# Performance work log

Measured on AMD Instinct MI355X. Metric: run time of the kernel, lower is better.

## Reference

```python
import jax, jax.numpy as jnp
import numpy as np

EMBED_DIM = 768
ATTN_DIM = 64


def setup_inputs() -> dict:
    key = jax.random.key(0)
    k1, k2, k3, k4 = jax.random.split(key, 4)
    embedded = jax.random.normal(k1, (4, 4096, EMBED_DIM), dtype=jnp.float32)
    scale = 1.0 / np.sqrt(EMBED_DIM)
    Wq = jax.random.normal(k2, (EMBED_DIM, ATTN_DIM), dtype=jnp.float32) * scale
    Wk = jax.random.normal(k3, (EMBED_DIM, ATTN_DIM), dtype=jnp.float32) * scale
    Wv = jax.random.normal(k4, (EMBED_DIM, ATTN_DIM), dtype=jnp.float32) * scale
    return {"embedded": embedded, "Wq": Wq, "Wk": Wk, "Wv": Wv}


def reference(embedded, Wq, Wk, Wv):
    # Linear projections (bias=False): [B, S, A]
    q = jnp.einsum("bse,ea->bsa", embedded, Wq)
    k = jnp.einsum("bse,ea->bsa", embedded, Wk)
    v = jnp.einsum("bse,ea->bsa", embedded, Wv)
    # Full [B, S, S] score matrix, as in the original naive implementation
    scores = jnp.einsum("bqa,bka->bqk", q, k) / jnp.sqrt(jnp.float32(ATTN_DIM))
    seq_len = embedded.shape[-2]
    causal = jnp.tril(jnp.ones((seq_len, seq_len), dtype=bool))
    scores = jnp.where(causal, scores, -jnp.inf)
    weights = jax.nn.softmax(scores, axis=-1)
    output = jnp.einsum("bqk,bka->bqa", weights, v)
    # torch.round(output, decimals=4)
    return jnp.round(output * 1e4) / 1e4
```

## Files before the change

### kernel.cpp

```cpp
#include <hip/hip_runtime.h>

#define NB 4
#define SEQ 4096
#define EMB 768
#define AD 64
#define BS (NB*SEQ)
#define CHK 16

typedef short short8 __attribute__((ext_vector_type(8)));
typedef float f32x4 __attribute__((ext_vector_type(4)));
typedef int   i32x2 __attribute__((ext_vector_type(2)));
typedef unsigned short u16;

__device__ __forceinline__ u16 f2bf(float f) {
  union { float f; unsigned u; } v; v.f = f;
  unsigned u = v.u;
  unsigned r = (u + 0x7FFFu + ((u >> 16) & 1u)) >> 16;
  return (u16)r;
}

__device__ __forceinline__ float bf2f(u16 b) {
  union { unsigned u; float f; } v; v.u = ((unsigned)b) << 16;
  return v.f;
}

__device__ __forceinline__ unsigned cvt_pk_bf16(float lo, float hi) {
  unsigned r;
  asm("v_cvt_pk_bf16_f32 %0, %1, %2" : "=v"(r) : "v"(lo), "v"(hi));
  return r;
}

__device__ __forceinline__ f32x4 mfma16(short8 a, short8 b, f32x4 c) {
  return __builtin_amdgcn_mfma_f32_16x16x32_bf16(a, b, c, 0, 0, 0);
}

__device__ __forceinline__ void gload16(const u16* g, u16* l) {
  __builtin_amdgcn_global_load_lds(
      (const __attribute__((address_space(1))) unsigned*)g,
      (__attribute__((address_space(3))) unsigned*)l, 16, 0, 0);
}

__device__ __forceinline__ float xor16_max(float x) {
#if __has_builtin(__builtin_amdgcn_permlane16_swap)
  i32x2 r = __builtin_amdgcn_permlane16_swap(__float_as_int(x), __float_as_int(x), false, false);
  return fmaxf(__int_as_float(r[0]), __int_as_float(r[1]));
#else
  return fmaxf(x, __shfl_xor(x, 16));
#endif
}
__device__ __forceinline__ float xor16_sum(float x) {
#if __has_builtin(__builtin_amdgcn_permlane16_swap)
  i32x2 r = __builtin_amdgcn_permlane16_swap(__float_as_int(x), __float_as_int(x), false, false);
  return __int_as_float(r[0]) + __int_as_float(r[1]);
#else
  return x + __shfl_xor(x, 16);
#endif
}
__device__ __forceinline__ float xor32_max(float x) {
#if __has_builtin(__builtin_amdgcn_permlane32_swap)
  i32x2 r = __builtin_amdgcn_permlane32_swap(__float_as_int(x), __float_as_int(x), false, false);
  return fmaxf(__int_as_float(r[0]), __int_as_float(r[1]));
#else
  return fmaxf(x, __shfl_xor(x, 32));
#endif
}
__device__ __forceinline__ float xor32_sum(float x) {
#if __has_builtin(__builtin_amdgcn_permlane32_swap)
  i32x2 r = __builtin_amdgcn_permlane32_swap(__float_as_int(x), __float_as_int(x), false, false);
  return __int_as_float(r[0]) + __int_as_float(r[1]);
#else
  return x + __shfl_xor(x, 32);
#endif
}

__global__ void wt_kernel(const float* __restrict__ Wq, const float* __restrict__ Wk,
                          const float* __restrict__ Wv, u16* __restrict__ Wt) {
  int idx = blockIdx.x * 256 + threadIdx.x;
  if (idx >= 3 * AD * EMB) return;
  int m   = idx / (AD * EMB);
  int rem = idx - m * (AD * EMB);
  int col = rem / EMB;
  int e   = rem - col * EMB;
  const float* W = (m == 0) ? Wq : (m == 1) ? Wk : Wv;
  Wt[idx] = f2bf(W[e * AD + col]);
}

__global__ __launch_bounds__(512) void proj_kernel(const float* __restrict__ emb,
                                                   const u16* __restrict__ Wt,
                                                   u16* __restrict__ Q, u16* __restrict__ K,
                                                   u16* __restrict__ Vt) {
  const int w = threadIdx.x >> 6;
  const int lane = threadIdx.x & 63;
  const int g = lane >> 4, c = lane & 15;
  const int wr = w & 1;
  const int cq = w >> 1;
  const int rbase = blockIdx.x * 32;

  __shared__ __align__(16) char ebuf[2][2][4096];
  __shared__ __align__(16) char wbuf[2][2][12288];
  __shared__ u16 t[32][65];

  const int r8 = lane >> 3, j8 = lane & 7;
  const int c4 = lane >> 2, j4 = lane & 3;

  f32x4 acc[3];
#pragma unroll
  for (int fi = 0; fi < 3; ++fi)
#pragma unroll
    for (int r = 0; r < 4; ++r) acc[fi][r] = 0.f;

#define PSTAGE(bufi, kk, kt) do {                                              \
    { const int col = w * 16 + c4;                                             \
      const int kc = (col & 3) ^ ((col >> 2) & 3);                             \
      gload16(Wt + (size_t)col * EMB + (kt) * 32 + ((j4 ^ kc) << 3),           \
              (u16*)(wbuf[bufi][kk] + w * 1024)); }                            \
    if (w < 4) {                                                               \
      gload16((const u16*)(emb + (size_t)(rbase + w * 8 + r8) * EMB            \
                           + (kt) * 32 + ((j8 ^ r8) << 2)),                    \
              (u16*)(ebuf[bufi][kk] + w * 1024));                              \
    } else {                                                                   \
      const int col = (4 + w) * 16 + c4;                                       \
      const int kc = (col & 3) ^ ((col >> 2) & 3);                             \
      gload16(Wt + (size_t)col * EMB + (kt) * 32 + ((j4 ^ kc) << 3),           \
              (u16*)(wbuf[bufi][kk] + (4 + w) * 1024));                        \
    }                                                                          \
  } while (0)

  PSTAGE(0, 0, 0);
  PSTAGE(0, 1, 1);
  __syncthreads();

  int cur = 0;
  for (int it = 0; it < 12; ++it) {
    if (it + 1 < 12) {
      PSTAGE(cur ^ 1, 0, 2 * it + 2);
      PSTAGE(cur ^ 1, 1, 2 * it + 3);
    }

#pragma unroll
    for (int kk = 0; kk < 2; ++kk) {
      const char* eb = ebuf[cur][kk];
      const int arow = (wr * 16 + c) * 128;
      const int sw = (c & 7) << 4;
      float4 fa0 = *(const float4*)(eb + arow + ((g * 32) ^ sw));
      float4 fa1 = *(const float4*)(eb + arow + ((g * 32 + 16) ^ sw));
      union { unsigned u[4]; short8 v; } uu;
      uu.u[0] = cvt_pk_bf16(fa0.x, fa0.y);
      uu.u[1] = cvt_pk_bf16(fa0.z, fa0.w);
      uu.u[2] = cvt_pk_bf16(fa1.x, fa1.y);
      uu.u[3] = cvt_pk_bf16(fa1.z, fa1.w);
      const short8 af = uu.v;

      const char* wb = wbuf[cur][kk];
#pragma unroll
      for (int fi = 0; fi < 3; ++fi) {
        const int fg = cq * 3 + fi;
        const int col = (fg >> 2) * 64 + (fg & 3) * 16 + c;
        const int kc = (col & 3) ^ ((col >> 2) & 3);
        short8 bf = *(const short8*)(wb + col * 64 + ((g ^ kc) << 4));
        acc[fi] = mfma16(af, bf, acc[fi]);
      }
    }

    __syncthreads();
    cur ^= 1;
  }

#pragma unroll
  for (int fi = 0; fi < 3; ++fi) {
    const int fg = cq * 3 + fi;
    const int m = fg >> 2, cf = fg & 3;
    const int col = cf * 16 + c;
#pragma unroll
    for (int r = 0; r < 4; ++r) {
      const int rloc = wr * 16 + g * 4 + r;
      const size_t grow = (size_t)(rbase + rloc);
      const float v = acc[fi][r];
      if (m == 0)      Q[grow * AD + col] = f2bf(v * 0.125f);
      else if (m == 1) K[grow * AD + col] = f2bf(v);
      else             t[rloc][col] = f2bf(v);
    }
  }
  __syncthreads();
  const int bb = blockIdx.x >> 7;
  const int sb = (blockIdx.x & 127) * 32;
  const int s = threadIdx.x & 31;
  const int d0 = threadIdx.x >> 5;
#pragma unroll
  for (int it = 0; it < 4; ++it) {
    const int d = it * 16 + d0;
    Vt[(size_t)(bb * AD + d) * SEQ + sb + s] = t[s][d];
  }
#undef PSTAGE
}

__global__ __launch_bounds__(256, 3) void flash_part(const u16* __restrict__ Q,
                                                     const u16* __restrict__ K,
                                                     const u16* __restrict__ Vt,
                                                     u16* __restrict__ opart,
                                                     float* __restrict__ ml) {
  const int bx = blockIdx.x;
  const int b = bx & 3;
  const int u = bx >> 2;
  int bq, c;
  if (u < 16)       { bq = 16 + u;        c = 0; }
  else if (u < 32)  { bq = 32 + (u - 16); c = 0; }
  else if (u < 48)  { bq = 32 + (u - 32); c = 1; }
  else if (u < 64)  { bq = 48 + (u - 48); c = 0; }
  else if (u < 80)  { bq = 48 + (u - 64); c = 1; }
  else if (u < 96)  { bq = 48 + (u - 80); c = 2; }
  else { int d = u - 96; bq = (d >> 4) * 16 + 15 - (d & 15); c = d >> 4; }
  const int t0 = c * CHK;
  const int tend = (c == (bq >> 4)) ? (bq + 1) : (t0 + CHK);

  const int w = threadIdx.x >> 6;
  const int lane = threadIdx.x & 63;
  const int g = lane >> 4, cl = lane & 15;
  const int r8 = lane >> 3, c16 = lane & 7;
  const int q0 = bq * 64 + w * 16;

  const u16* Qb = Q + (size_t)b * SEQ * AD;
  const u16* Kb = K + (size_t)b * SEQ * AD;
  const u16* Vb = Vt + (size_t)b * AD * SEQ;

  __shared__ __align__(16) u16 kbuf[2][64 * 64];
  __shared__ __align__(16) u16 vbuf[2][64 * 64];
  __shared__ __align__(16) u16 plds_all[4][16 * 64];
  char* plds = (char*)plds_all[w];
  const int swz = (cl & 7) << 4;
  const int prow = cl * 128;
  const int fsw = (cl & 7);

  const short8 qf0 = *(const short8*)(Qb + (size_t)(q0 + cl) * AD + g * 8);
  const short8 qf1 = *(const short8*)(Qb + (size_t)(q0 + cl) * AD + 32 + g * 8);

  float mrow = -INFINITY, lrow = 0.f;
  f32x4 o[4];
#pragma unroll
  for (int cf = 0; cf < 4; cf++)
#pragma unroll
    for (int r = 0; r < 4; r++) o[cf][r] = 0.f;

#define STAGE(bufi, tt) do {                                                   \
    const int kvb = (tt) * 64;                                                 \
    const int row0 = w * 16 + r8, row1 = w * 16 + 8 + r8;                      \
    gload16(Kb + (size_t)(kvb + row0) * AD + ((c16 ^ r8) << 3),                \
            &kbuf[bufi][(w * 16) * 64]);                                       \
    gload16(Kb + (size_t)(kvb + row1) * AD + ((c16 ^ r8) << 3),                \
            &kbuf[bufi][(w * 16 + 8) * 64]);                                   \
    gload16(Vb + (size_t)row0 * SEQ + kvb + ((c16 ^ r8) << 3),                 \
            &vbuf[bufi][(w * 16) * 64]);                                       \
    gload16(Vb + (size_t)row1 * SEQ + kvb + ((c16 ^ r8) << 3),                 \
            &vbuf[bufi][(w * 16 + 8) * 64]);                                   \
  } while (0)

  STAGE(0, t0);
  __syncthreads();

  int cur = 0;
  for (int t = t0; t < tend; ++t) {
    const int kv0 = t * 64;
    if (t + 1 < tend) STAGE(cur ^ 1, t + 1);

    const char* kb = (const char*)kbuf[cur];
    const char* vb = (const char*)vbuf[cur];

    short8 kf0[4], kf1[4];
#pragma unroll
    for (int cf = 0; cf < 4; cf++) {
      const int kr = (cf * 16 + cl) * 128;
      kf0[cf] = *(const short8*)(kb + kr + ((g ^ fsw) << 4));
      kf1[cf] = *(const short8*)(kb + kr + (((4 + g) ^ fsw) << 4));
    }

    f32x4 s4[4];
#pragma unroll
    for (int cf = 0; cf < 4; cf++) {
      f32x4 z; z[0] = z[1] = z[2] = z[3] = 0.f;
      z = mfma16(kf0[cf], qf0, z);
      s4[cf] = mfma16(kf1[cf], qf1, z);
    }

    if (t == bq) {
#pragma unroll
      for (int cf = 0; cf < 4; cf++) {
        const int kvb2 = kv0 + cf * 16 + g * 4;
#pragma unroll
        for (int r = 0; r < 4; r++)
          s4[cf][r] = (kvb2 + r <= q0 + cl) ? s4[cf][r] : -INFINITY;
      }
    }

    float tm[4];
#pragma unroll
    for (int cf = 0; cf < 4; cf++)
      tm[cf] = fmaxf(fmaxf(s4[cf][0], s4[cf][1]), fmaxf(s4[cf][2], s4[cf][3]));
    float mt = fmaxf(fmaxf(tm[0], tm[1]), fmaxf(tm[2], tm[3]));
    mt = xor16_max(mt);
    mt = xor32_max(mt);

    if (!__all(mt <= mrow + 8.0f)) {
      const float mn = fmaxf(mrow, mt);
      const float corr = __expf(mrow - mn);
      mrow = mn;
      lrow *= corr;
      float cb[4];
#pragma unroll
      for (int r = 0; r < 4; r++) cb[r] = __shfl(corr, g * 20 + r);
#pragma unroll
      for (int cf = 0; cf < 4; cf++) {
        o[cf][0] *= cb[0]; o[cf][1] *= cb[1];
        o[cf][2] *= cb[2]; o[cf][3] *= cb[3];
      }
    }

    float rs = 0.f;
#pragma unroll
    for (int cf = 0; cf < 4; cf++) {
      const float p0 = __expf(s4[cf][0] - mrow);
      const float p1 = __expf(s4[cf][1] - mrow);
      const float p2 = __expf(s4[cf][2] - mrow);
      const float p3 = __expf(s4[cf][3] - mrow);
      rs += (p0 + p1) + (p2 + p3);
      uint2 val;
      val.x = cvt_pk_bf16(p0, p1);
      val.y = cvt_pk_bf16(p2, p3);
      *(uint2*)(plds + prow + (((cf * 32) + (g * 8)) ^ swz)) = val;
    }
    rs = xor16_sum(rs);
    rs = xor32_sum(rs);
    lrow += rs;

    asm volatile("" ::: "memory");

#pragma unroll
    for (int f = 0; f < 2; ++f) {
      const short8 pf = *(const short8*)(plds + prow + ((f * 64 + g * 16) ^ swz));
#pragma unroll
      for (int cf = 0; cf < 4; cf++) {
        const int vr = (cf * 16 + cl) * 128;
        const short8 vfa = *(const short8*)(vb + vr + (((f * 4 + g) ^ fsw) << 4));
        o[cf] = mfma16(pf, vfa, o[cf]);
      }
    }

    __syncthreads();
    cur ^= 1;
  }

  const int qg = bq * 4 + w;
  const int k2 = qg >> 6;
  const int slot = b * 640 + 32 * k2 * (k2 + 1) + (qg & 63) * (k2 + 1) + c;

  if (lane < 16) {
    ml[(size_t)slot * 32 + cl * 2 + 0] = mrow;
    ml[(size_t)slot * 32 + cl * 2 + 1] = lrow;
  }
#pragma unroll
  for (int cf = 0; cf < 4; cf++)
#pragma unroll
    for (int r = 0; r < 4; r++)
      opart[(size_t)slot * 1024 + (g * 4 + r) * 64 + cf * 16 + cl] = f2bf(o[cf][r]);
#undef STAGE
}

__global__ __launch_bounds__(256) void combine_kernel(const u16* __restrict__ opart,
                                                      const float* __restrict__ ml,
                                                      float* __restrict__ out) {
  const int tid = threadIdx.x;
  const int row = blockIdx.x * 16 + (tid >> 4);
  const int d = (tid & 15) * 4;
  const int b = row >> 12;
  const int rowb = row & 4095;
  const int qg = rowb >> 4;
  const int r = rowb & 15;
  const int k2 = qg >> 6;
  const int nc = k2 + 1;
  const int sbase = b * 640 + 32 * k2 * (k2 + 1) + (qg & 63) * nc;

  float M = -INFINITY;
  float ms[4], ls[4];
  for (int cc = 0; cc < nc; cc++) {
    ms[cc] = ml[(size_t)(sbase + cc) * 32 + r * 2 + 0];
    ls[cc] = ml[(size_t)(sbase + cc) * 32 + r * 2 + 1];
    M = fmaxf(M, ms[cc]);
  }
  float L = 0.f;
  float4 acc = {0.f, 0.f, 0.f, 0.f};
  for (int cc = 0; cc < nc; cc++) {
    const float wgt = __expf(ms[cc] - M);
    L += ls[cc] * wgt;
    ushort4 ov = *(const ushort4*)(opart + (size_t)(sbase + cc) * 1024 + r * 64 + d);
    acc.x += bf2f(ov.x) * wgt; acc.y += bf2f(ov.y) * wgt;
    acc.z += bf2f(ov.z) * wgt; acc.w += bf2f(ov.w) * wgt;
  }
  const float inv = 1.0f / L;
  float4 res;
  res.x = rintf(acc.x * inv * 1.0e4f) * 1.0e-4f;
  res.y = rintf(acc.y * inv * 1.0e4f) * 1.0e-4f;
  res.z = rintf(acc.z * inv * 1.0e4f) * 1.0e-4f;
  res.w = rintf(acc.w * inv * 1.0e4f) * 1.0e-4f;
  *(float4*)(out + (size_t)row * AD + d) = res;
}

extern "C" void kernel_launch(void* const* d_in, const int* in_sizes, int n_in,
                              void* d_out, int out_size, void* d_ws, size_t ws_size,
                              hipStream_t stream) {
  const float* emb = (const float*)d_in[0];
  const float* Wq  = (const float*)d_in[1];
  const float* Wk  = (const float*)d_in[2];
  const float* Wv  = (const float*)d_in[3];
  float* out = (float*)d_out;

  char* ws = (char*)d_ws;
  u16* Wt = (u16*)ws;
  u16* Q  = (u16*)(ws + 294912);
  u16* K  = Q + (size_t)BS * AD;
  u16* Vt = K + (size_t)BS * AD;
  u16* opart = (u16*)(ws + 294912 + 3 * (size_t)BS * AD * 2);
  float* ml  = (float*)(ws + 294912 + 3 * (size_t)BS * AD * 2
                        + (size_t)2560 * 1024 * 2);

  wt_kernel<<<(3 * AD * EMB + 255) / 256, 256, 0, stream>>>(Wq, Wk, Wv, Wt);
  proj_kernel<<<BS / 32, 512, 0, stream>>>(emb, Wt, Q, K, Vt);
  flash_part<<<640, 256, 0, stream>>>(Q, K, Vt, opart, ml);
  combine_kernel<<<BS / 16, 256, 0, stream>>>(opart, ml, out);
}
```

Before: 57.95 us.

## Process two 16-row query tiles per wave in flash kernel with 2 waves per block

```diff
diff --git a/kernel.cpp b/kernel.cpp
--- a/kernel.cpp
+++ b/kernel.cpp
@@ -194,7 +194,7 @@
 #undef PSTAGE
 }
 
-__global__ __launch_bounds__(256, 3) void flash_part(const u16* __restrict__ Q,
+__global__ __launch_bounds__(128, 2) void flash_part(const u16* __restrict__ Q,
                                                      const u16* __restrict__ K,
                                                      const u16* __restrict__ Vt,
                                                      u16* __restrict__ opart,
@@ -217,7 +217,7 @@
   const int lane = threadIdx.x & 63;
   const int g = lane >> 4, cl = lane & 15;
   const int r8 = lane >> 3, c16 = lane & 7;
-  const int q0 = bq * 64 + w * 16;
+  const int q0 = bq * 64 + w * 32;
 
   const u16* Qb = Q + (size_t)b * SEQ * AD;
   const u16* Kb = K + (size_t)b * SEQ * AD;
@@ -225,33 +225,36 @@
 
   __shared__ __align__(16) u16 kbuf[2][64 * 64];
   __shared__ __align__(16) u16 vbuf[2][64 * 64];
-  __shared__ __align__(16) u16 plds_all[4][16 * 64];
-  char* plds = (char*)plds_all[w];
+  __shared__ __align__(16) u16 plds_all[2][2][16 * 64];
+  char* pldsA = (char*)plds_all[w][0];
+  char* pldsB = (char*)plds_all[w][1];
   const int swz = (cl & 7) << 4;
   const int prow = cl * 128;
   const int fsw = (cl & 7);
 
-  const short8 qf0 = *(const short8*)(Qb + (size_t)(q0 + cl) * AD + g * 8);
-  const short8 qf1 = *(const short8*)(Qb + (size_t)(q0 + cl) * AD + 32 + g * 8);
-
-  float mrow = -INFINITY, lrow = 0.f;
-  f32x4 o[4];
+  const short8 qf0a = *(const short8*)(Qb + (size_t)(q0 + cl) * AD + g * 8);
+  const short8 qf1a = *(const short8*)(Qb + (size_t)(q0 + cl) * AD + 32 + g * 8);
+  const short8 qf0b = *(const short8*)(Qb + (size_t)(q0 + 16 + cl) * AD + g * 8);
+  const short8 qf1b = *(const short8*)(Qb + (size_t)(q0 + 16 + cl) * AD + 32 + g * 8);
+
+  float mrow_a = -INFINITY, lrow_a = 0.f;
+  float mrow_b = -INFINITY, lrow_b = 0.f;
+  f32x4 oa[4], ob[4];
 #pragma unroll
   for (int cf = 0; cf < 4; cf++)
 #pragma unroll
-    for (int r = 0; r < 4; r++) o[cf][r] = 0.f;
+    for (int r = 0; r < 4; r++) { oa[cf][r] = 0.f; ob[cf][r] = 0.f; }
 
 #define STAGE(bufi, tt) do {                                                   \
     const int kvb = (tt) * 64;                                                 \
-    const int row0 = w * 16 + r8, row1 = w * 16 + 8 + r8;                      \
-    gload16(Kb + (size_t)(kvb + row0) * AD + ((c16 ^ r8) << 3),                \
-            &kbuf[bufi][(w * 16) * 64]);                                       \
-    gload16(Kb + (size_t)(kvb + row1) * AD + ((c16 ^ r8) << 3),                \
-            &kbuf[bufi][(w * 16 + 8) * 64]);                                   \
-    gload16(Vb + (size_t)row0 * SEQ + kvb + ((c16 ^ r8) << 3),                 \
-            &vbuf[bufi][(w * 16) * 64]);                                       \
-    gload16(Vb + (size_t)row1 * SEQ + kvb + ((c16 ^ r8) << 3),                 \
-            &vbuf[bufi][(w * 16 + 8) * 64]);                                   \
+    _Pragma("unroll")                                                          \
+    for (int rr = 0; rr < 4; ++rr) {                                           \
+      const int row0 = w * 32 + rr * 8 + r8;                                   \
+      gload16(Kb + (size_t)(kvb + row0) * AD + ((c16 ^ r8) << 3),              \
+              &kbuf[bufi][(w * 32 + rr * 8) * 64]);                            \
+      gload16(Vb + (size_t)row0 * SEQ + kvb + ((c16 ^ r8) << 3),               \
+              &vbuf[bufi][(w * 32 + rr * 8) * 64]);                            \
+    }                                                                          \
   } while (0)
 
   STAGE(0, t0);
@@ -273,12 +276,15 @@
       kf1[cf] = *(const short8*)(kb + kr + (((4 + g) ^ fsw) << 4));
     }
 
-    f32x4 s4[4];
+    f32x4 s4a[4], s4b[4];
 #pragma unroll
     for (int cf = 0; cf < 4; cf++) {
-      f32x4 z; z[0] = z[1] = z[2] = z[3] = 0.f;
-      z = mfma16(kf0[cf], qf0, z);
-      s4[cf] = mfma16(kf1[cf], qf1, z);
+      f32x4 za; za[0] = za[1] = za[2] = za[3] = 0.f;
+      f32x4 zb; zb[0] = zb[1] = zb[2] = zb[3] = 0.f;
+      za = mfma16(kf0[cf], qf0a, za);
+      s4a[cf] = mfma16(kf1[cf], qf1a, za);
+      zb = mfma16(kf0[cf], qf0b, zb);
+      s4b[cf] = mfma16(kf1[cf], qf1b, zb);
     }
 
     if (t == bq) {
@@ -286,61 +292,83 @@
       for (int cf = 0; cf < 4; cf++) {
         const int kvb2 = kv0 + cf * 16 + g * 4;
 #pragma unroll
-        for (int r = 0; r < 4; r++)
-          s4[cf][r] = (kvb2 + r <= q0 + cl) ? s4[cf][r] : -INFINITY;
+        for (int r = 0; r < 4; r++) {
+          s4a[cf][r] = (kvb2 + r <= q0 + cl)      ? s4a[cf][r] : -INFINITY;
+          s4b[cf][r] = (kvb2 + r <= q0 + 16 + cl) ? s4b[cf][r] : -INFINITY;
+        }
       }
     }
 
-    float tm[4];
-#pragma unroll
-    for (int cf = 0; cf < 4; cf++)
-      tm[cf] = fmaxf(fmaxf(s4[cf][0], s4[cf][1]), fmaxf(s4[cf][2], s4[cf][3]));
-    float mt = fmaxf(fmaxf(tm[0], tm[1]), fmaxf(tm[2], tm[3]));
-    mt = xor16_max(mt);
-    mt = xor32_max(mt);
-
-    if (!__all(mt <= mrow + 8.0f)) {
-      const float mn = fmaxf(mrow, mt);
-      const float corr = __expf(mrow - mn);
-      mrow = mn;
-      lrow *= corr;
-      float cb[4];
-#pragma unroll
-      for (int r = 0; r < 4; r++) cb[r] = __shfl(corr, g * 20 + r);
+    float tma[4], tmb[4];
+#pragma unroll
+    for (int cf = 0; cf < 4; cf++) {
+      tma[cf] = fmaxf(fmaxf(s4a[cf][0], s4a[cf][1]), fmaxf(s4a[cf][2], s4a[cf][3]));
+      tmb[cf] = fmaxf(fmaxf(s4b[cf][0], s4b[cf][1]), fmaxf(s4b[cf][2], s4b[cf][3]));
+    }
+    float mta = fmaxf(fmaxf(tma[0], tma[1]), fmaxf(tma[2], tma[3]));
+    float mtb = fmaxf(fmaxf(tmb[0], tmb[1]), fmaxf(tmb[2], tmb[3]));
+    mta = xor16_max(mta); mta = xor32_max(mta);
+    mtb = xor16_max(mtb); mtb = xor32_max(mtb);
+
+    if (!__all((mta <= mrow_a + 8.0f) && (mtb <= mrow_b + 8.0f))) {
+      const float mna = fmaxf(mrow_a, mta);
+      const float corr_a = __expf(mrow_a - mna);
+      mrow_a = mna; lrow_a *= corr_a;
+      const float mnb = fmaxf(mrow_b, mtb);
+      const float corr_b = __expf(mrow_b - mnb);
+      mrow_b = mnb; lrow_b *= corr_b;
+      float cba[4], cbb[4];
+#pragma unroll
+      for (int r = 0; r < 4; r++) {
+        cba[r] = __shfl(corr_a, g * 20 + r);
+        cbb[r] = __shfl(corr_b, g * 20 + r);
+      }
 #pragma unroll
       for (int cf = 0; cf < 4; cf++) {
-        o[cf][0] *= cb[0]; o[cf][1] *= cb[1];
-        o[cf][2] *= cb[2]; o[cf][3] *= cb[3];
+        oa[cf][0] *= cba[0]; oa[cf][1] *= cba[1];
+        oa[cf][2] *= cba[2]; oa[cf][3] *= cba[3];
+        ob[cf][0] *= cbb[0]; ob[cf][1] *= cbb[1];
+        ob[cf][2] *= cbb[2]; ob[cf][3] *= cbb[3];
       }
     }
 
-    float rs = 0.f;
+    float rsa = 0.f, rsb = 0.f;
 #pragma unroll
     for (int cf = 0; cf < 4; cf++) {
-      const float p0 = __expf(s4[cf][0] - mrow);
-      const float p1 = __expf(s4[cf][1] - mrow);
-      const float p2 = __expf(s4[cf][2] - mrow);
-      const float p3 = __expf(s4[cf][3] - mrow);
-      rs += (p0 + p1) + (p2 + p3);
-      uint2 val;
-      val.x = cvt_pk_bf16(p0, p1);
-      val.y = cvt_pk_bf16(p2, p3);
-      *(uint2*)(plds + prow + (((cf * 32) + (g * 8)) ^ swz)) = val;
-    }
-    rs = xor16_sum(rs);
-    rs = xor32_sum(rs);
-    lrow += rs;
+      const float a0 = __expf(s4a[cf][0] - mrow_a);
+      const float a1 = __expf(s4a[cf][1] - mrow_a);
+      const float a2 = __expf(s4a[cf][2] - mrow_a);
+      const float a3 = __expf(s4a[cf][3] - mrow_a);
+      rsa += (a0 + a1) + (a2 + a3);
+      uint2 va;
+      va.x = cvt_pk_bf16(a0, a1);
+      va.y = cvt_pk_bf16(a2, a3);
+      *(uint2*)(pldsA + prow + (((cf * 32) + (g * 8)) ^ swz)) = va;
+      const float b0 = __expf(s4b[cf][0] - mrow_b);
+      const float b1 = __expf(s4b[cf][1] - mrow_b);
+      const float b2 = __expf(s4b[cf][2] - mrow_b);
+      const float b3 = __expf(s4b[cf][3] - mrow_b);
+      rsb += (b0 + b1) + (b2 + b3);
+      uint2 vbw;
+      vbw.x = cvt_pk_bf16(b0, b1);
+      vbw.y = cvt_pk_bf16(b2, b3);
+      *(uint2*)(pldsB + prow + (((cf * 32) + (g * 8)) ^ swz)) = vbw;
+    }
+    rsa = xor16_sum(rsa); rsa = xor32_sum(rsa); lrow_a += rsa;
+    rsb = xor16_sum(rsb); rsb = xor32_sum(rsb); lrow_b += rsb;
 
     asm volatile("" ::: "memory");
 
 #pragma unroll
     for (int f = 0; f < 2; ++f) {
-      const short8 pf = *(const short8*)(plds + prow + ((f * 64 + g * 16) ^ swz));
+      const short8 pfA = *(const short8*)(pldsA + prow + ((f * 64 + g * 16) ^ swz));
+      const short8 pfB = *(const short8*)(pldsB + prow + ((f * 64 + g * 16) ^ swz));
 #pragma unroll
       for (int cf = 0; cf < 4; cf++) {
         const int vr = (cf * 16 + cl) * 128;
         const short8 vfa = *(const short8*)(vb + vr + (((f * 4 + g) ^ fsw) << 4));
-        o[cf] = mfma16(pf, vfa, o[cf]);
+        oa[cf] = mfma16(pfA, vfa, oa[cf]);
+        ob[cf] = mfma16(pfB, vfa, ob[cf]);
       }
     }
 
@@ -348,19 +376,25 @@
     cur ^= 1;
   }
 
-  const int qg = bq * 4 + w;
-  const int k2 = qg >> 6;
-  const int slot = b * 640 + 32 * k2 * (k2 + 1) + (qg & 63) * (k2 + 1) + c;
+  const int qga = bq * 4 + w * 2;
+  const int qgb = qga + 1;
+  const int k2 = qga >> 6;
+  const int slota = b * 640 + 32 * k2 * (k2 + 1) + (qga & 63) * (k2 + 1) + c;
+  const int slotb = b * 640 + 32 * k2 * (k2 + 1) + (qgb & 63) * (k2 + 1) + c;
 
   if (lane < 16) {
-    ml[(size_t)slot * 32 + cl * 2 + 0] = mrow;
-    ml[(size_t)slot * 32 + cl * 2 + 1] = lrow;
+    ml[(size_t)slota * 32 + cl * 2 + 0] = mrow_a;
+    ml[(size_t)slota * 32 + cl * 2 + 1] = lrow_a;
+    ml[(size_t)slotb * 32 + cl * 2 + 0] = mrow_b;
+    ml[(size_t)slotb * 32 + cl * 2 + 1] = lrow_b;
   }
 #pragma unroll
   for (int cf = 0; cf < 4; cf++)
 #pragma unroll
-    for (int r = 0; r < 4; r++)
-      opart[(size_t)slot * 1024 + (g * 4 + r) * 64 + cf * 16 + cl] = f2bf(o[cf][r]);
+    for (int r = 0; r < 4; r++) {
+      opart[(size_t)slota * 1024 + (g * 4 + r) * 64 + cf * 16 + cl] = f2bf(oa[cf][r]);
+      opart[(size_t)slotb * 1024 + (g * 4 + r) * 64 + cf * 16 + cl] = f2bf(ob[cf][r]);
+    }
 #undef STAGE
 }
 
@@ -423,6 +457,6 @@
 
   wt_kernel<<<(3 * AD * EMB + 255) / 256, 256, 0, stream>>>(Wq, Wk, Wv, Wt);
   proj_kernel<<<BS / 32, 512, 0, stream>>>(emb, Wt, Q, K, Vt);
-  flash_part<<<640, 256, 0, stream>>>(Q, K, Vt, opart, ml);
+  flash_part<<<640, 128, 0, stream>>>(Q, K, Vt, opart, ml);
   combine_kernel<<<BS / 16, 256, 0, stream>>>(opart, ml, out);
 }
```

New measurement: 64.92 us. 1.12x slower.
